# Optimization experiments

Hardware: AMD Instinct MI355X
Metric: run time of the kernel (lower is better)

## Reference

```python
import jax, jax.numpy as jnp
import numpy as np

B, T, E, H = 2, 2048, 1024, 16
D = E // H
K_KEEP = 391
RECENCY = 64
SCALE = D ** -0.5


def setup_inputs() -> dict:
    key = jax.random.key(0)
    k1, k2, k3 = jax.random.split(key, 3)
    x = jax.random.normal(k1, (B, T, E), jnp.float32)
    W_attn = jax.random.normal(k2, (3 * E, E), jnp.float32) * 0.02  # torch Linear weight [out,in]
    W_proj = jax.random.normal(k3, (E, E), jnp.float32) * 0.02
    return {"x": x, "W_attn": W_attn, "W_proj": W_proj}


def reference(x, W_attn, W_proj):
    b, t, c = x.shape
    qkv = x @ W_attn.T                      # [B,T,3E]
    q, k, v = jnp.split(qkv, 3, axis=-1)
    to_heads = lambda u: u.reshape(b, t, H, D).transpose(0, 2, 1, 3)  # [B,H,T,D]
    q, k, v = to_heads(q), to_heads(k), to_heads(v)

    # first pass: causal attention weights for importance scoring
    scores = jnp.einsum('bhqd,bhkd->bhqk', q, k) * SCALE
    causal = jnp.tril(jnp.ones((t, t), dtype=bool))
    scores = jnp.where(causal, scores, -jnp.inf)
    attn_w = jax.nn.softmax(scores, axis=-1)

    # mean importance over query dim, force-keep recent tokens
    imp = attn_w.mean(axis=2)               # [B,H,T]
    imp = imp.at[:, :, -RECENCY:].set(1.0)

    # top-k token selection per (batch, head)
    _, idx = jax.lax.top_k(imp, K_KEEP)     # [B,H,K]

    # gather pruned K/V
    K_keep = jnp.take_along_axis(k, idx[..., None], axis=2)  # [B,H,K,D]
    V_keep = jnp.take_along_axis(v, idx[..., None], axis=2)

    # second attention pass over pruned keys (no causal mask, matches legacy code)
    s2 = jnp.einsum('bhqd,bhkd->bhqk', q, K_keep) * SCALE
    a2 = jax.nn.softmax(s2, axis=-1)
    out = jnp.einsum('bhqk,bhkd->bhqd', a2, V_keep)          # [B,H,T,D]

    out = out.transpose(0, 2, 1, 3).reshape(b, t, c)
    return out @ W_proj.T
```

## Files before the change

kernel.cpp:

```cpp
#include <hip/hip_runtime.h>
#include <hip/hip_bf16.h>


#define TT 2048
#define EE 1024
#define HH 16
#define DD 64
#define KKEEP 391
#define REC 64
#define NBH 32
#define QSCALE 0.125f
#define KPAD 448

typedef short bf16x8 __attribute__((ext_vector_type(8)));
typedef _Float16 f16x8 __attribute__((ext_vector_type(8)));
typedef float f32x4 __attribute__((ext_vector_type(4)));

#define WAIT_VM(N) asm volatile("s_waitcnt vmcnt(" #N ")" ::: "memory")
#define WAIT_LGKM0 asm volatile("s_waitcnt lgkmcnt(0)" ::: "memory")
#define BAR() __builtin_amdgcn_s_barrier()

static __device__ inline unsigned short bf_rn(float x) {
  unsigned u = __float_as_uint(x);
  unsigned r = u + 0x7fffu + ((u >> 16) & 1u);
  return (unsigned short)(r >> 16);
}
static __device__ inline float bf_up(unsigned short h) {
  return __uint_as_float((unsigned)h << 16);
}
static __device__ inline unsigned pkf16(float a, float b) {
  union { _Float16 h[2]; unsigned u; } t;
  t.h[0] = (_Float16)a; t.h[1] = (_Float16)b; return t.u;
}
static __device__ inline void glds16(const void* g, void* l) {
  __builtin_amdgcn_global_load_lds(
      (const __attribute__((address_space(1))) void*)g,
      (__attribute__((address_space(3))) void*)l, 16, 0, 0);
}

static __device__ inline void split4(const float* __restrict__ src,
                                     unsigned short* __restrict__ ho,
                                     unsigned short* __restrict__ lo_, int i)
{
  float4 v = *reinterpret_cast<const float4*>(&src[i]);
  ushort4 hh, ll;
  float f;
  hh.x = bf_rn(v.x); f = bf_up(hh.x); ll.x = bf_rn(v.x - f);
  hh.y = bf_rn(v.y); f = bf_up(hh.y); ll.y = bf_rn(v.y - f);
  hh.z = bf_rn(v.z); f = bf_up(hh.z); ll.z = bf_rn(v.z - f);
  hh.w = bf_rn(v.w); f = bf_up(hh.w); ll.w = bf_rn(v.w - f);
  *reinterpret_cast<ushort4*>(&ho[i]) = hh;
  *reinterpret_cast<ushort4*>(&lo_[i]) = ll;
}

__global__ __launch_bounds__(256) void split_kernel(
    const float* __restrict__ src, unsigned short* __restrict__ ho,
    unsigned short* __restrict__ lo_, int n)
{
  int i = (blockIdx.x * 256 + threadIdx.x) * 4;
  const int stride = gridDim.x * 1024;
  for (; i < n; i += stride) split4(src, ho, lo_, i);
}

__global__ __launch_bounds__(256) void split2_kernel(
    const float* __restrict__ x, const float* __restrict__ wa,
    unsigned short* __restrict__ xh, unsigned short* __restrict__ xl,
    unsigned short* __restrict__ wh, unsigned short* __restrict__ wl)
{
  const int n1 = 4096 * 1024, n2 = 3072 * 1024;
  int i = (blockIdx.x * 256 + threadIdx.x) * 4;
  const int stride = gridDim.x * 1024;
  for (; i < n1 + n2; i += stride) {
    if (i < n1) split4(x, xh, xl, i);
    else        split4(wa, wh, wl, i - n1);
  }
}

template<bool VB, int MODE>
__global__ __launch_bounds__(256) void gemm_pipe(
    const unsigned short* __restrict__ Ah, const unsigned short* __restrict__ Al,
    const unsigned short* __restrict__ Bh, const unsigned short* __restrict__ Bl,
    float* __restrict__ Cc, unsigned short* __restrict__ Qho, unsigned short* __restrict__ Qlo,
    unsigned short* __restrict__ Kho, unsigned short* __restrict__ Klo,
    float* __restrict__ Vo, int M, int N, int Kd, int nOff)
{
  __shared__ __align__(16) unsigned short Ahs[2][128 * 32];
  __shared__ __align__(16) unsigned short Bhs[2][128 * 32];
  __shared__ __align__(16) unsigned short Als[VB ? 1 : 2][128 * 32];
  __shared__ __align__(16) unsigned short Bls[VB ? 1 : 2][128 * 32];
  const int tid = threadIdx.x;
  const int m0 = blockIdx.y * 128, n0 = nOff + blockIdx.x * 128;
  const int w = tid >> 6, lane = tid & 63;
  const int wm = w >> 1, wn = w & 1;
  const int l15 = lane & 15, l4 = lane >> 4;

  size_t gA[2], gB[2]; int ldso[2];
#pragma unroll
  for (int s = 0; s < 2; s++) {
    int seg = w * 2 + s;
    int r = seg * 16 + (lane >> 2);
    int kb = (lane & 3) ^ ((r >> 1) & 3);
    gA[s] = (size_t)(m0 + r) * Kd + kb * 8;
    gB[s] = (size_t)(n0 + r) * Kd + kb * 8;
    ldso[s] = seg * 512;
  }
  auto STAGE = [&](int bb, int k0) {
#pragma unroll
    for (int s = 0; s < 2; s++) {
      glds16(&Ah[gA[s] + k0], &Ahs[bb][ldso[s]]);
      glds16(&Bh[gB[s] + k0], &Bhs[bb][ldso[s]]);
      if (!VB) {
        glds16(&Al[gA[s] + k0], &Als[bb][ldso[s]]);
        glds16(&Bl[gB[s] + k0], &Bls[bb][ldso[s]]);
      }
    }
  };

  f32x4 acc[4][4] = {};

  STAGE(0, 0);
  STAGE(1, 32);
  int cur = 0;
  for (int k0 = 0; k0 < Kd; k0 += 32) {
    if (k0 + 32 < Kd) { if (VB) WAIT_VM(4); else WAIT_VM(8); }
    else WAIT_VM(0);
    BAR();
    bf16x8 ah[4], al[4], bh[4], bl[4];
#pragma unroll
    for (int i = 0; i < 4; i++) {
      int ar = wm * 64 + i * 16 + l15;
      int aoff = ar * 32 + ((l4 ^ ((ar >> 1) & 3)) * 8);
      ah[i] = *reinterpret_cast<const bf16x8*>(&Ahs[cur][aoff]);
      int br = wn * 64 + i * 16 + l15;
      int boff = br * 32 + ((l4 ^ ((br >> 1) & 3)) * 8);
      bh[i] = *reinterpret_cast<const bf16x8*>(&Bhs[cur][boff]);
      if (!VB) {
        al[i] = *reinterpret_cast<const bf16x8*>(&Als[cur][aoff]);
        bl[i] = *reinterpret_cast<const bf16x8*>(&Bls[cur][boff]);
      }
    }
#pragma unroll
    for (int i = 0; i < 4; i++)
#pragma unroll
      for (int j = 0; j < 4; j++) {
        acc[i][j] = __builtin_amdgcn_mfma_f32_16x16x32_bf16(ah[i], bh[j], acc[i][j], 0, 0, 0);
        if (!VB) {
          acc[i][j] = __builtin_amdgcn_mfma_f32_16x16x32_bf16(ah[i], bl[j], acc[i][j], 0, 0, 0);
          acc[i][j] = __builtin_amdgcn_mfma_f32_16x16x32_bf16(al[i], bh[j], acc[i][j], 0, 0, 0);
        }
      }
    WAIT_LGKM0;
    BAR();
    if (k0 + 64 < Kd) STAGE(cur, k0 + 64);
    cur ^= 1;
  }

  if (MODE == 0) {
#pragma unroll
    for (int i = 0; i < 4; i++) {
      int mrow0 = m0 + wm * 64 + i * 16 + l4 * 4;
#pragma unroll
      for (int j = 0; j < 4; j++) {
        int ncol = n0 + wn * 64 + j * 16 + l15;
#pragma unroll
        for (int r = 0; r < 4; r++)
          Cc[(size_t)(mrow0 + r) * N + ncol] = acc[i][j][r];
      }
    }
  } else if (VB) {
#pragma unroll
    for (int j = 0; j < 4; j++) {
      int n = n0 + wn * 64 + j * 16 + l15;
      int rr = n & 1023;
      int h = rr >> 6, d0 = rr & 63;
#pragma unroll
      for (int i = 0; i < 4; i++) {
        int mrow0 = m0 + wm * 64 + i * 16 + l4 * 4;
#pragma unroll
        for (int r = 0; r < 4; r++) {
          int m = mrow0 + r;
          int b = m >> 11, t = m & 2047;
          Vo[((size_t)((b * HH + h) * TT + t)) * DD + d0] = acc[i][j][r];
        }
      }
    }
  } else {
#pragma unroll
    for (int j = 0; j < 4; j++) {
      int n = n0 + wn * 64 + j * 16 + l15;
      int p = n >> 10, rr = n & 1023;
      int h = rr >> 6, d0 = rr & 63;
#pragma unroll
      for (int i = 0; i < 4; i++) {
        int mrow0 = m0 + wm * 64 + i * 16 + l4 * 4;
#pragma unroll
        for (int r = 0; r < 4; r++) {
          int m = mrow0 + r;
          int b = m >> 11, t = m & 2047;
          size_t idx = ((size_t)((b * HH + h) * TT + t)) * DD + d0;
          float v = acc[i][j][r];
          unsigned short hi_ = bf_rn(v);
          unsigned short lo2 = bf_rn(v - bf_up(hi_));
          if (p == 0) { Qho[idx] = hi_; Qlo[idx] = lo2; }
          else        { Kho[idx] = hi_; Klo[idx] = lo2; }
        }
      }
    }
  }
}

__global__ __launch_bounds__(512) void importance5_kernel(
    const unsigned short* __restrict__ Qh, const unsigned short* __restrict__ Ql,
    const unsigned short* __restrict__ Kh, const unsigned short* __restrict__ Kl,
    float* __restrict__ part)
{
  const int bh = blockIdx.x;
  const int rt = blockIdx.z ? (15 - (int)blockIdx.y) : (int)blockIdx.y;
  const int slab = ((int)blockIdx.y << 1) | (int)blockIdx.z;
  const int row0 = rt * 128;
  const int nch = rt + 1;
  const int tid = threadIdx.x;
  const int w = tid >> 6, lane = tid & 63;
  const int wm = w >> 1, wn = w & 1;
  const int l15 = lane & 15, l4 = lane >> 4;
  __shared__ __align__(16) unsigned short Khs[2][128 * 64];
  __shared__ __align__(16) unsigned short Kls[2][128 * 64];
  __shared__ float csw[8 * 128];
  __shared__ float rsb[2 * 128];

  int krow[2], kkb[2], klds[2];
#pragma unroll
  for (int s = 0; s < 2; s++) {
    int seg = w * 2 + s;
    int r = seg * 8 + (lane >> 3);
    int k8 = lane & 7;
    krow[s] = r; kkb[s] = k8 ^ (r & 7); klds[s] = seg * 512;
  }
  auto STAGEK1 = [&](int bb, int ci) {
#pragma unroll
    for (int s = 0; s < 2; s++) {
      size_t ga = ((size_t)(bh * TT + ci * 128 + krow[s])) * DD + kkb[s] * 8;
      glds16(&Kh[ga], &Khs[bb][klds[s]]);
    }
  };
  auto STAGEK2 = [&](int bb, int ci) {
#pragma unroll
    for (int s = 0; s < 2; s++) {
      size_t ga = ((size_t)(bh * TT + ci * 128 + krow[s])) * DD + kkb[s] * 8;
      glds16(&Kh[ga], &Khs[bb][klds[s]]);
      glds16(&Kl[ga], &Kls[bb][klds[s]]);
    }
  };

  bf16x8 aq[2][2], aql[2][2];
#pragma unroll
  for (int ks = 0; ks < 2; ks++)
#pragma unroll
    for (int i = 0; i < 2; i++) {
      int ar = wm * 32 + i * 16 + l15;
      size_t ga = ((size_t)(bh * TT + row0 + ar)) * DD + (ks * 4 + l4) * 8;
      aq[ks][i]  = *reinterpret_cast<const bf16x8*>(&Qh[ga]);
      aql[ks][i] = *reinterpret_cast<const bf16x8*>(&Ql[ga]);
    }

  float rsum[2][4];
#pragma unroll
  for (int i = 0; i < 2; i++)
#pragma unroll
    for (int r = 0; r < 4; r++) rsum[i][r] = 0.f;
  float invl[2][4];

  STAGEK1(0, 0);
  if (nch > 1) STAGEK1(1, 1);
  int cur = 0;
  for (int ci = 0; ci < nch; ci++) {
    if (ci + 1 < nch) WAIT_VM(2); else WAIT_VM(0);
    BAR();
    f32x4 acc[2][4] = {};
#pragma unroll
    for (int ks = 0; ks < 2; ks++) {
#pragma unroll
      for (int j = 0; j < 4; j++) {
        int br = wn * 64 + j * 16 + l15;
        int off = br * 64 + (((ks * 4 + l4) ^ (br & 7)) * 8);
        bf16x8 bh_ = *reinterpret_cast<const bf16x8*>(&Khs[cur][off]);
#pragma unroll
        for (int i = 0; i < 2; i++)
          acc[i][j] = __builtin_amdgcn_mfma_f32_16x16x32_bf16(aq[ks][i], bh_, acc[i][j], 0, 0, 0);
      }
    }
    const bool diag = (ci == rt);
#pragma unroll
    for (int i = 0; i < 2; i++)
#pragma unroll
      for (int r = 0; r < 4; r++) {
        int row = row0 + wm * 32 + i * 16 + l4 * 4 + r;
        float s = 0.f;
#pragma unroll
        for (int j = 0; j < 4; j++) {
          int key = ci * 128 + wn * 64 + j * 16 + l15;
          float p = __expf(acc[i][j][r] * QSCALE);
          if (diag && key > row) p = 0.f;
          s += p;
        }
        rsum[i][r] += s;
      }
    WAIT_LGKM0;
    BAR();
    if (ci + 2 < nch) STAGEK1(cur, ci + 2);
    cur ^= 1;
  }
#pragma unroll
  for (int i = 0; i < 2; i++)
#pragma unroll
    for (int r = 0; r < 4; r++) {
      float v = rsum[i][r];
      v += __shfl_xor(v, 1); v += __shfl_xor(v, 2);
      v += __shfl_xor(v, 4); v += __shfl_xor(v, 8);
      rsum[i][r] = v;
    }
  __syncthreads();
  if (l15 == 0) {
#pragma unroll
    for (int i = 0; i < 2; i++)
#pragma unroll
      for (int r = 0; r < 4; r++)
        rsb[wn * 128 + wm * 32 + i * 16 + l4 * 4 + r] = rsum[i][r];
  }
  __syncthreads();
#pragma unroll
  for (int i = 0; i < 2; i++)
#pragma unroll
    for (int r = 0; r < 4; r++) {
      int rl = wm * 32 + i * 16 + l4 * 4 + r;
      invl[i][r] = 1.0f / (rsb[rl] + rsb[128 + rl]);
    }

  STAGEK2(0, 0);
  if (nch > 1) STAGEK2(1, 1);
  cur = 0;
  for (int ci = 0; ci < nch; ci++) {
    if (ci + 1 < nch) WAIT_VM(4); else WAIT_VM(0);
    BAR();
    f32x4 acc[2][4] = {};
#pragma unroll
    for (int ks = 0; ks < 2; ks++) {
#pragma unroll
      for (int j = 0; j < 4; j++) {
        int br = wn * 64 + j * 16 + l15;
        int off = br * 64 + (((ks * 4 + l4) ^ (br & 7)) * 8);
        bf16x8 bh_ = *reinterpret_cast<const bf16x8*>(&Khs[cur][off]);
        bf16x8 bl_ = *reinterpret_cast<const bf16x8*>(&Kls[cur][off]);
#pragma unroll
        for (int i = 0; i < 2; i++) {
          acc[i][j] = __builtin_amdgcn_mfma_f32_16x16x32_bf16(aq[ks][i], bh_, acc[i][j], 0, 0, 0);
          acc[i][j] = __builtin_amdgcn_mfma_f32_16x16x32_bf16(aq[ks][i], bl_, acc[i][j], 0, 0, 0);
          acc[i][j] = __builtin_amdgcn_mfma_f32_16x16x32_bf16(aql[ks][i], bh_, acc[i][j], 0, 0, 0);
        }
      }
    }
    const bool diag = (ci == rt);
    float cp[4];
#pragma unroll
    for (int j = 0; j < 4; j++) cp[j] = 0.f;
#pragma unroll
    for (int i = 0; i < 2; i++)
#pragma unroll
      for (int r = 0; r < 4; r++) {
        int row = row0 + wm * 32 + i * 16 + l4 * 4 + r;
        float il = invl[i][r];
#pragma unroll
        for (int j = 0; j < 4; j++) {
          int key = ci * 128 + wn * 64 + j * 16 + l15;
          float p = __expf(acc[i][j][r] * QSCALE) * il;
          if (diag && key > row) p = 0.f;
          cp[j] += p;
        }
      }
#pragma unroll
    for (int j = 0; j < 4; j++) {
      float v = cp[j];
      v += __shfl_xor(v, 16); v += __shfl_xor(v, 32);
      cp[j] = v;
    }
    WAIT_LGKM0;
    BAR();
    if (ci + 2 < nch) STAGEK2(cur, ci + 2);
    if (l4 == 0) {
#pragma unroll
      for (int j = 0; j < 4; j++)
        csw[w * 128 + wn * 64 + j * 16 + l15] = cp[j];
    }
    WAIT_LGKM0;
    BAR();
    if (tid < 128) {
      int wnc = tid >> 6;
      float s = csw[(0 * 2 + wnc) * 128 + tid] + csw[(1 * 2 + wnc) * 128 + tid] +
                csw[(2 * 2 + wnc) * 128 + tid] + csw[(3 * 2 + wnc) * 128 + tid];
      part[((size_t)(bh * 16 + slab)) * 2048 + ci * 128 + tid] = s;
    }
    cur ^= 1;
  }
}

__global__ __launch_bounds__(256) void topk_gather_kernel(
    const float* __restrict__ part,
    const unsigned short* __restrict__ Kh, const unsigned short* __restrict__ Kl,
    const float* __restrict__ V,
    unsigned short* __restrict__ Kf, unsigned short* __restrict__ Vt)
{
  const int bh = blockIdx.x, tid = threadIdx.x;
  const int lane = tid & 63, w = tid >> 6;
  __shared__ int redi[4];
  __shared__ int stot;
  __shared__ int base[256];
  __shared__ int idxb[KKEEP];
  unsigned u[8];
#pragma unroll
  for (int k = 0; k < 8; k++) {
    int e = tid * 8 + k;
    float s = 0.f;
#pragma unroll
    for (int p = 0; p < 16; p++) {
      int rtp = (p & 1) ? 15 - (p >> 1) : (p >> 1);
      if (e < (rtp + 1) * 128) s += part[((size_t)(bh * 16 + p)) * 2048 + e];
    }
    float v = (e >= TT - REC) ? 3.0e3f : s;
    u[k] = __float_as_uint(v);
  }
  unsigned lo = 0u, hi = 0x7f800000u;
  for (int it = 0; it < 31; it++) {
    unsigned mid = lo + ((hi - lo + 1) >> 1);
    int c = 0;
#pragma unroll
    for (int k = 0; k < 8; k++) c += (u[k] >= mid) ? 1 : 0;
#pragma unroll
    for (int off = 1; off <= 32; off <<= 1) c += __shfl_xor(c, off);
    if (lane == 0) redi[w] = c;
    __syncthreads();
    int tot = redi[0] + redi[1] + redi[2] + redi[3];
    if (tot >= KKEEP) lo = mid; else hi = mid - 1;
    __syncthreads();
  }
  const unsigned vstar = lo;
  int cgt = 0, ceq = 0;
#pragma unroll
  for (int k = 0; k < 8; k++) { cgt += (u[k] > vstar) ? 1 : 0; ceq += (u[k] == vstar) ? 1 : 0; }
  base[tid] = cgt; __syncthreads();
  if (tid == 0) {
    int run = 0;
    for (int i = 0; i < 256; i++) { int t = base[i]; base[i] = run; run += t; }
    stot = run;
  }
  __syncthreads();
  int off1 = base[tid];
#pragma unroll
  for (int k = 0; k < 8; k++)
    if (u[k] > vstar) idxb[off1++] = tid * 8 + k;
  __syncthreads();
  base[tid] = ceq; __syncthreads();
  if (tid == 0) {
    int run = 0;
    for (int i = 0; i < 256; i++) { int t = base[i]; base[i] = run; run += t; }
  }
  __syncthreads();
  int off2 = stot + base[tid];
#pragma unroll
  for (int k = 0; k < 8; k++)
    if (u[k] == vstar) { if (off2 < KKEEP) idxb[off2] = tid * 8 + k; off2++; }
  __syncthreads();
  for (int f = tid; f < KPAD * 8; f += 256) {
    int kk = f >> 3, c8 = f & 7;
    union { _Float16 h[8]; uint4 v; } o;
#pragma unroll
    for (int j = 0; j < 8; j++) o.h[j] = (_Float16)0.f;
    if (kk < KKEEP) {
      int sr = idxb[kk];
      bf16x8 hv = *reinterpret_cast<const bf16x8*>(&Kh[((size_t)(bh * TT + sr)) * DD + c8 * 8]);
      bf16x8 lv = *reinterpret_cast<const bf16x8*>(&Kl[((size_t)(bh * TT + sr)) * DD + c8 * 8]);
#pragma unroll
      for (int j = 0; j < 8; j++)
        o.h[j] = (_Float16)(bf_up((unsigned short)hv[j]) + bf_up((unsigned short)lv[j]));
    }
    *reinterpret_cast<uint4*>(&Kf[((size_t)(bh * KPAD) + kk) * DD + c8 * 8]) = o.v;
  }
  for (int f = tid; f < KPAD * 8; f += 256) {
    int kk = f >> 3, d8 = f & 7;
    float vv[8];
#pragma unroll
    for (int j = 0; j < 8; j++) vv[j] = 0.f;
    if (kk < KKEEP) {
      int sr = idxb[kk];
      float4 a = *reinterpret_cast<const float4*>(&V[((size_t)(bh * TT + sr)) * DD + d8 * 8]);
      float4 b = *reinterpret_cast<const float4*>(&V[((size_t)(bh * TT + sr)) * DD + d8 * 8 + 4]);
      vv[0] = a.x; vv[1] = a.y; vv[2] = a.z; vv[3] = a.w;
      vv[4] = b.x; vv[5] = b.y; vv[6] = b.z; vv[7] = b.w;
    }
#pragma unroll
    for (int j = 0; j < 8; j++) {
      union { _Float16 h; unsigned short s; } t;
      t.h = (_Float16)vv[j];
      Vt[((size_t)(bh * DD) + d8 * 8 + j) * KPAD + kk] = t.s;
    }
  }
}

__global__ __launch_bounds__(256) void attn4_kernel(
    const unsigned short* __restrict__ Qh, const unsigned short* __restrict__ Ql,
    const unsigned short* __restrict__ Kf, const unsigned short* __restrict__ Vt,
    unsigned short* __restrict__ AOh, unsigned short* __restrict__ AOl)
{
  const int rt = blockIdx.y, bh = blockIdx.x;
  const int tid = threadIdx.x;
  const int w = tid >> 6, lane = tid & 63;
  const int l15 = lane & 15, l4 = lane >> 4;
  __shared__ __align__(16) unsigned short Qs[64 * 64];
  __shared__ __align__(16) unsigned short Ks[2][64 * 64];
  __shared__ __align__(16) unsigned short Vs[2][64 * 64];
  __shared__ float LDSo[4][64][16];
  const int row0 = rt * 64;

  int srow[2], skb[2], slds[2];
#pragma unroll
  for (int s = 0; s < 2; s++) {
    int seg = w * 2 + s;
    int r = seg * 8 + (lane >> 3);
    int k8 = lane & 7;
    srow[s] = r; skb[s] = k8 ^ (r & 7); slds[s] = seg * 512;
  }
  auto STAGEA = [&](int bb, int ci) {
#pragma unroll
    for (int s = 0; s < 2; s++) {
      glds16(&Kf[((size_t)(bh * KPAD) + ci * 64 + srow[s]) * DD + skb[s] * 8], &Ks[bb][slds[s]]);
      glds16(&Vt[((size_t)(bh * DD) + srow[s]) * KPAD + ci * 64 + skb[s] * 8], &Vs[bb][slds[s]]);
    }
  };

#pragma unroll
  for (int it = 0; it < 2; it++) {
    int idx = it * 256 + tid;
    int r = idx >> 3, k8 = idx & 7;
    size_t ga = ((size_t)(bh * TT + row0 + r)) * DD + k8 * 8;
    bf16x8 hv = *reinterpret_cast<const bf16x8*>(&Qh[ga]);
    bf16x8 lv = *reinterpret_cast<const bf16x8*>(&Ql[ga]);
    union { _Float16 h[8]; uint4 v; } q16;
#pragma unroll
    for (int j = 0; j < 8; j++)
      q16.h[j] = (_Float16)(bf_up((unsigned short)hv[j]) + bf_up((unsigned short)lv[j]));
    *reinterpret_cast<uint4*>(&Qs[r * 64 + ((k8 ^ (r & 7)) * 8)]) = q16.v;
  }
  STAGEA(0, 0);
  STAGEA(1, 1);
  WAIT_LGKM0;
  BAR();
  f16x8 bq[2];
#pragma unroll
  for (int ks = 0; ks < 2; ks++) {
    int br = w * 16 + l15;
    bq[ks] = *reinterpret_cast<const f16x8*>(&Qs[br * 64 + (((ks * 4 + l4) ^ (br & 7)) * 8)]);
  }

  f32x4 acc_o[4] = {};
  float rsum = 0.f;
  int cur = 0;

  for (int ci = 0; ci < 7; ci++) {
    if (ci + 1 < 7) WAIT_VM(4); else WAIT_VM(0);
    BAR();
    f32x4 accs[4] = {};
#pragma unroll
    for (int ks = 0; ks < 2; ks++) {
#pragma unroll
      for (int i = 0; i < 4; i++) {
        int kr = i * 16 + l15;
        f16x8 af = *reinterpret_cast<const f16x8*>(&Ks[cur][kr * 64 + (((ks * 4 + l4) ^ (kr & 7)) * 8)]);
        accs[i] = __builtin_amdgcn_mfma_f32_16x16x32_f16(af, bq[ks], accs[i], 0, 0, 0);
      }
    }
    float p[4][4];
#pragma unroll
    for (int i = 0; i < 4; i++)
#pragma unroll
      for (int r = 0; r < 4; r++) {
        int gk = ci * 64 + i * 16 + l4 * 4 + r;
        float pp = __expf(accs[i][r] * QSCALE);
        if (gk >= KKEEP) pp = 0.f;
        p[i][r] = pp;
        rsum += pp;
      }
    unsigned pkU[4][2];
#pragma unroll
    for (int i = 0; i < 4; i++) {
      pkU[i][0] = pkf16(p[i][0], p[i][1]);
      pkU[i][1] = pkf16(p[i][2], p[i][3]);
    }
#pragma unroll
    for (int ks = 0; ks < 2; ks++) {
      union { f16x8 h; unsigned u[4]; } bp;
#pragma unroll
      for (int wp = 0; wp < 4; wp++) {
        int src = ((l4 & 1) * 2 + (wp >> 1)) * 16 + l15;
        unsigned v0 = (unsigned)__shfl((int)pkU[ks * 2][wp & 1], src);
        unsigned v1 = (unsigned)__shfl((int)pkU[ks * 2 + 1][wp & 1], src);
        bp.u[wp] = (l4 & 2) ? v1 : v0;
      }
#pragma unroll
      for (int i = 0; i < 4; i++) {
        int dr = i * 16 + l15;
        f16x8 av = *reinterpret_cast<const f16x8*>(&Vs[cur][dr * 64 + (((ks * 4 + l4) ^ (dr & 7)) * 8)]);
        acc_o[i] = __builtin_amdgcn_mfma_f32_16x16x32_f16(av, bp.h, acc_o[i], 0, 0, 0);
      }
    }
    WAIT_LGKM0;
    BAR();
    if (ci + 2 < 7) STAGEA(cur, ci + 2);
    cur ^= 1;
  }
  rsum += __shfl_xor(rsum, 16);
  rsum += __shfl_xor(rsum, 32);
  float inv = 1.0f / rsum;
#pragma unroll
  for (int i = 0; i < 4; i++)
#pragma unroll
    for (int r = 0; r < 4; r++)
      LDSo[w][i * 16 + l4 * 4 + r][l15] = acc_o[i][r] * inv;
  __syncthreads();
  const int b = bh >> 4, h = bh & 15;
#pragma unroll
  for (int uu = 0; uu < 2; uu++) {
    int u = uu * 64 + lane;
    int q = u >> 3, dc = u & 7;
    int row = row0 + w * 16 + q;
    union { unsigned short s[8]; uint4 v; } sh, sl;
#pragma unroll
    for (int j = 0; j < 8; j++) {
      float v = LDSo[w][dc * 8 + j][q];
      unsigned short hh = bf_rn(v);
      sh.s[j] = hh;
      sl.s[j] = bf_rn(v - bf_up(hh));
    }
    size_t addr = ((size_t)(b * TT + row)) * EE + h * DD + dc * 8;
    *reinterpret_cast<uint4*>(&AOh[addr]) = sh.v;
    *reinterpret_cast<uint4*>(&AOl[addr]) = sl.v;
  }
}

extern "C" void kernel_launch(void* const* d_in, const int* in_sizes, int n_in,
                              void* d_out, int out_size, void* d_ws, size_t ws_size,
                              hipStream_t stream)
{
  const float* x     = (const float*)d_in[0];
  const float* Wattn = (const float*)d_in[1];
  const float* Wproj = (const float*)d_in[2];
  float* out = (float*)d_out;
  float* ws  = (float*)d_ws;

  const size_t SZQ = (size_t)NBH * TT * DD;
  const size_t SZK = (size_t)NBH * KPAD * DD;
  float* Vb   = ws;
  float* part = Vb + SZQ;
  unsigned short* Kf  = (unsigned short*)(part + (size_t)NBH * 16 * TT);
  unsigned short* Vt  = Kf + SZK;
  unsigned short* Qhp = Vt + SZK;
  unsigned short* Qlp = Qhp + SZQ;
  unsigned short* Khp = Qlp + SZQ;
  unsigned short* Klp = Khp + SZQ;
  unsigned short* xh  = Klp + SZQ;
  unsigned short* xl  = xh + (size_t)4096 * 1024;
  unsigned short* Wh  = xl + (size_t)4096 * 1024;
  unsigned short* Wl  = Wh + (size_t)3072 * 1024;
  unsigned short* AOh = xh;
  unsigned short* AOl = xl;
  unsigned short* Ph  = Wh;
  unsigned short* Pl  = Ph + (size_t)1024 * 1024;

  const size_t needB =
      ((size_t)SZQ + (size_t)NBH * 16 * TT) * 4 +
      ((size_t)2 * SZK + (size_t)4 * SZQ + (size_t)2 * 4096 * 1024 + (size_t)2 * 3072 * 1024) * 2;
  if (ws_size < needB) return;

  split2_kernel<<<1024, 256, 0, stream>>>(x, Wattn, xh, xl, Wh, Wl);
  gemm_pipe<false, 1><<<dim3(16, 32), 256, 0, stream>>>(xh, xl, Wh, Wl, nullptr,
      Qhp, Qlp, Khp, Klp, nullptr, 4096, 3072, 1024, 0);
  gemm_pipe<true, 1><<<dim3(8, 32), 256, 0, stream>>>(xh, xl, Wh, Wl, nullptr,
      nullptr, nullptr, nullptr, nullptr, Vb, 4096, 3072, 1024, 2048);
  split_kernel<<<256, 256, 0, stream>>>(Wproj, Ph, Pl, 1024 * 1024);
  importance5_kernel<<<dim3(NBH, 8, 2), 512, 0, stream>>>(Qhp, Qlp, Khp, Klp, part);
  topk_gather_kernel<<<NBH, 256, 0, stream>>>(part, Khp, Klp, Vb, Kf, Vt);
  attn4_kernel<<<dim3(NBH, 32), 256, 0, stream>>>(Qhp, Qlp, Kf, Vt, AOh, AOl);
  gemm_pipe<false, 0><<<dim3(8, 32), 256, 0, stream>>>(AOh, AOl, Ph, Pl, out,
      nullptr, nullptr, nullptr, nullptr, nullptr, 4096, 1024, 1024, 0);
}
```

Baseline: 261.9 us.

## Merge QKV GEMMs into one 512-thread kernel and shrink importance key chunks

```diff
diff --git a/kernel.cpp b/kernel.cpp
--- a/kernel.cpp
+++ b/kernel.cpp
@@ -76,77 +76,72 @@
   }
 }
 
-template<bool VB, int MODE>
-__global__ __launch_bounds__(256) void gemm_pipe(
+template<int MODE>
+__global__ __launch_bounds__(512, 4) void gemm512(
     const unsigned short* __restrict__ Ah, const unsigned short* __restrict__ Al,
     const unsigned short* __restrict__ Bh, const unsigned short* __restrict__ Bl,
     float* __restrict__ Cc, unsigned short* __restrict__ Qho, unsigned short* __restrict__ Qlo,
     unsigned short* __restrict__ Kho, unsigned short* __restrict__ Klo,
-    float* __restrict__ Vo, int M, int N, int Kd, int nOff)
+    float* __restrict__ Vo, int M, int N, int Kd)
 {
   __shared__ __align__(16) unsigned short Ahs[2][128 * 32];
   __shared__ __align__(16) unsigned short Bhs[2][128 * 32];
-  __shared__ __align__(16) unsigned short Als[VB ? 1 : 2][128 * 32];
-  __shared__ __align__(16) unsigned short Bls[VB ? 1 : 2][128 * 32];
+  __shared__ __align__(16) unsigned short Als[2][128 * 32];
+  __shared__ __align__(16) unsigned short Bls[2][128 * 32];
   const int tid = threadIdx.x;
-  const int m0 = blockIdx.y * 128, n0 = nOff + blockIdx.x * 128;
+  const int m0 = blockIdx.y * 128, n0 = blockIdx.x * 128;
   const int w = tid >> 6, lane = tid & 63;
-  const int wm = w >> 1, wn = w & 1;
+  const int wm = w >> 2, wn = w & 3;
   const int l15 = lane & 15, l4 = lane >> 4;
-
-  size_t gA[2], gB[2]; int ldso[2];
-#pragma unroll
-  for (int s = 0; s < 2; s++) {
-    int seg = w * 2 + s;
-    int r = seg * 16 + (lane >> 2);
-    int kb = (lane & 3) ^ ((r >> 1) & 3);
-    gA[s] = (size_t)(m0 + r) * Kd + kb * 8;
-    gB[s] = (size_t)(n0 + r) * Kd + kb * 8;
-    ldso[s] = seg * 512;
-  }
+  const bool vblk = (MODE == 1) && (blockIdx.x >= 16);
+
+  const int sr = w * 16 + (lane >> 2);
+  const int skb = (lane & 3) ^ ((sr >> 1) & 3);
+  const size_t gA = (size_t)(m0 + sr) * Kd + skb * 8;
+  const size_t gB = (size_t)(n0 + sr) * Kd + skb * 8;
+  const int ldw = w * 512;
+
   auto STAGE = [&](int bb, int k0) {
-#pragma unroll
-    for (int s = 0; s < 2; s++) {
-      glds16(&Ah[gA[s] + k0], &Ahs[bb][ldso[s]]);
-      glds16(&Bh[gB[s] + k0], &Bhs[bb][ldso[s]]);
-      if (!VB) {
-        glds16(&Al[gA[s] + k0], &Als[bb][ldso[s]]);
-        glds16(&Bl[gB[s] + k0], &Bls[bb][ldso[s]]);
-      }
+    glds16(&Ah[gA + k0], &Ahs[bb][ldw]);
+    glds16(&Bh[gB + k0], &Bhs[bb][ldw]);
+    if (!vblk) {
+      glds16(&Al[gA + k0], &Als[bb][ldw]);
+      glds16(&Bl[gB + k0], &Bls[bb][ldw]);
     }
   };
 
-  f32x4 acc[4][4] = {};
+  f32x4 acc[4][2] = {};
 
   STAGE(0, 0);
   STAGE(1, 32);
   int cur = 0;
   for (int k0 = 0; k0 < Kd; k0 += 32) {
-    if (k0 + 32 < Kd) { if (VB) WAIT_VM(4); else WAIT_VM(8); }
+    if (k0 + 32 < Kd) { if (vblk) WAIT_VM(2); else WAIT_VM(4); }
     else WAIT_VM(0);
     BAR();
-    bf16x8 ah[4], al[4], bh[4], bl[4];
+    bf16x8 ahf[4], alf[4], bhf[2], blf[2];
 #pragma unroll
     for (int i = 0; i < 4; i++) {
       int ar = wm * 64 + i * 16 + l15;
       int aoff = ar * 32 + ((l4 ^ ((ar >> 1) & 3)) * 8);
-      ah[i] = *reinterpret_cast<const bf16x8*>(&Ahs[cur][aoff]);
-      int br = wn * 64 + i * 16 + l15;
+      ahf[i] = *reinterpret_cast<const bf16x8*>(&Ahs[cur][aoff]);
+      if (!vblk) alf[i] = *reinterpret_cast<const bf16x8*>(&Als[cur][aoff]);
+    }
+#pragma unroll
+    for (int j = 0; j < 2; j++) {
+      int br = wn * 32 + j * 16 + l15;
       int boff = br * 32 + ((l4 ^ ((br >> 1) & 3)) * 8);
-      bh[i] = *reinterpret_cast<const bf16x8*>(&Bhs[cur][boff]);
-      if (!VB) {
-        al[i] = *reinterpret_cast<const bf16x8*>(&Als[cur][aoff]);
-        bl[i] = *reinterpret_cast<const bf16x8*>(&Bls[cur][boff]);
-      }
+      bhf[j] = *reinterpret_cast<const bf16x8*>(&Bhs[cur][boff]);
+      if (!vblk) blf[j] = *reinterpret_cast<const bf16x8*>(&Bls[cur][boff]);
     }
 #pragma unroll
     for (int i = 0; i < 4; i++)
 #pragma unroll
-      for (int j = 0; j < 4; j++) {
-        acc[i][j] = __builtin_amdgcn_mfma_f32_16x16x32_bf16(ah[i], bh[j], acc[i][j], 0, 0, 0);
-        if (!VB) {
-          acc[i][j] = __builtin_amdgcn_mfma_f32_16x16x32_bf16(ah[i], bl[j], acc[i][j], 0, 0, 0);
-          acc[i][j] = __builtin_amdgcn_mfma_f32_16x16x32_bf16(al[i], bh[j], acc[i][j], 0, 0, 0);
+      for (int j = 0; j < 2; j++) {
+        acc[i][j] = __builtin_amdgcn_mfma_f32_16x16x32_bf16(ahf[i], bhf[j], acc[i][j], 0, 0, 0);
+        if (!vblk) {
+          acc[i][j] = __builtin_amdgcn_mfma_f32_16x16x32_bf16(ahf[i], blf[j], acc[i][j], 0, 0, 0);
+          acc[i][j] = __builtin_amdgcn_mfma_f32_16x16x32_bf16(alf[i], bhf[j], acc[i][j], 0, 0, 0);
         }
       }
     WAIT_LGKM0;
@@ -160,34 +155,17 @@
     for (int i = 0; i < 4; i++) {
       int mrow0 = m0 + wm * 64 + i * 16 + l4 * 4;
 #pragma unroll
-      for (int j = 0; j < 4; j++) {
-        int ncol = n0 + wn * 64 + j * 16 + l15;
+      for (int j = 0; j < 2; j++) {
+        int ncol = n0 + wn * 32 + j * 16 + l15;
 #pragma unroll
         for (int r = 0; r < 4; r++)
           Cc[(size_t)(mrow0 + r) * N + ncol] = acc[i][j][r];
       }
     }
-  } else if (VB) {
-#pragma unroll
-    for (int j = 0; j < 4; j++) {
-      int n = n0 + wn * 64 + j * 16 + l15;
-      int rr = n & 1023;
-      int h = rr >> 6, d0 = rr & 63;
-#pragma unroll
-      for (int i = 0; i < 4; i++) {
-        int mrow0 = m0 + wm * 64 + i * 16 + l4 * 4;
-#pragma unroll
-        for (int r = 0; r < 4; r++) {
-          int m = mrow0 + r;
-          int b = m >> 11, t = m & 2047;
-          Vo[((size_t)((b * HH + h) * TT + t)) * DD + d0] = acc[i][j][r];
-        }
-      }
-    }
   } else {
 #pragma unroll
-    for (int j = 0; j < 4; j++) {
-      int n = n0 + wn * 64 + j * 16 + l15;
+    for (int j = 0; j < 2; j++) {
+      int n = n0 + wn * 32 + j * 16 + l15;
       int p = n >> 10, rr = n & 1023;
       int h = rr >> 6, d0 = rr & 63;
 #pragma unroll
@@ -199,17 +177,21 @@
           int b = m >> 11, t = m & 2047;
           size_t idx = ((size_t)((b * HH + h) * TT + t)) * DD + d0;
           float v = acc[i][j][r];
-          unsigned short hi_ = bf_rn(v);
-          unsigned short lo2 = bf_rn(v - bf_up(hi_));
-          if (p == 0) { Qho[idx] = hi_; Qlo[idx] = lo2; }
-          else        { Kho[idx] = hi_; Klo[idx] = lo2; }
+          if (p == 2) {
+            Vo[idx] = v;
+          } else {
+            unsigned short hi_ = bf_rn(v);
+            unsigned short lo2 = bf_rn(v - bf_up(hi_));
+            if (p == 0) { Qho[idx] = hi_; Qlo[idx] = lo2; }
+            else        { Kho[idx] = hi_; Klo[idx] = lo2; }
+          }
         }
       }
     }
   }
 }
 
-__global__ __launch_bounds__(512) void importance5_kernel(
+__global__ __launch_bounds__(512, 8) void importance6_kernel(
     const unsigned short* __restrict__ Qh, const unsigned short* __restrict__ Ql,
     const unsigned short* __restrict__ Kh, const unsigned short* __restrict__ Kl,
     float* __restrict__ part)
@@ -218,38 +200,26 @@
   const int rt = blockIdx.z ? (15 - (int)blockIdx.y) : (int)blockIdx.y;
   const int slab = ((int)blockIdx.y << 1) | (int)blockIdx.z;
   const int row0 = rt * 128;
-  const int nch = rt + 1;
+  const int nch = 2 * rt + 2;
   const int tid = threadIdx.x;
   const int w = tid >> 6, lane = tid & 63;
   const int wm = w >> 1, wn = w & 1;
   const int l15 = lane & 15, l4 = lane >> 4;
-  __shared__ __align__(16) unsigned short Khs[2][128 * 64];
-  __shared__ __align__(16) unsigned short Kls[2][128 * 64];
-  __shared__ float csw[8 * 128];
+  __shared__ __align__(16) unsigned short Khs[2][64 * 64];
+  __shared__ __align__(16) unsigned short Kls[2][64 * 64];
+  __shared__ float csw[8 * 32];
   __shared__ float rsb[2 * 128];
 
-  int krow[2], kkb[2], klds[2];
-#pragma unroll
-  for (int s = 0; s < 2; s++) {
-    int seg = w * 2 + s;
-    int r = seg * 8 + (lane >> 3);
-    int k8 = lane & 7;
-    krow[s] = r; kkb[s] = k8 ^ (r & 7); klds[s] = seg * 512;
-  }
+  const int kr = w * 8 + (lane >> 3);
+  const int sk8 = (lane & 7) ^ (kr & 7);
+  const int ldw = w * 512;
   auto STAGEK1 = [&](int bb, int ci) {
-#pragma unroll
-    for (int s = 0; s < 2; s++) {
-      size_t ga = ((size_t)(bh * TT + ci * 128 + krow[s])) * DD + kkb[s] * 8;
-      glds16(&Kh[ga], &Khs[bb][klds[s]]);
-    }
+    glds16(&Kh[((size_t)(bh * TT + ci * 64 + kr)) * DD + sk8 * 8], &Khs[bb][ldw]);
   };
   auto STAGEK2 = [&](int bb, int ci) {
-#pragma unroll
-    for (int s = 0; s < 2; s++) {
-      size_t ga = ((size_t)(bh * TT + ci * 128 + krow[s])) * DD + kkb[s] * 8;
-      glds16(&Kh[ga], &Khs[bb][klds[s]]);
-      glds16(&Kl[ga], &Kls[bb][klds[s]]);
-    }
+    size_t ga = ((size_t)(bh * TT + ci * 64 + kr)) * DD + sk8 * 8;
+    glds16(&Kh[ga], &Khs[bb][ldw]);
+    glds16(&Kl[ga], &Kls[bb][ldw]);
   };
 
   bf16x8 aq[2][2], aql[2][2];
@@ -271,17 +241,17 @@
   float invl[2][4];
 
   STAGEK1(0, 0);
-  if (nch > 1) STAGEK1(1, 1);
+  STAGEK1(1, 1);
   int cur = 0;
   for (int ci = 0; ci < nch; ci++) {
-    if (ci + 1 < nch) WAIT_VM(2); else WAIT_VM(0);
-    BAR();
-    f32x4 acc[2][4] = {};
+    if (ci + 1 < nch) WAIT_VM(1); else WAIT_VM(0);
+    BAR();
+    f32x4 acc[2][2] = {};
 #pragma unroll
     for (int ks = 0; ks < 2; ks++) {
 #pragma unroll
-      for (int j = 0; j < 4; j++) {
-        int br = wn * 64 + j * 16 + l15;
+      for (int j = 0; j < 2; j++) {
+        int br = wn * 32 + j * 16 + l15;
         int off = br * 64 + (((ks * 4 + l4) ^ (br & 7)) * 8);
         bf16x8 bh_ = *reinterpret_cast<const bf16x8*>(&Khs[cur][off]);
 #pragma unroll
@@ -289,22 +259,33 @@
           acc[i][j] = __builtin_amdgcn_mfma_f32_16x16x32_bf16(aq[ks][i], bh_, acc[i][j], 0, 0, 0);
       }
     }
-    const bool diag = (ci == rt);
-#pragma unroll
-    for (int i = 0; i < 2; i++)
-#pragma unroll
-      for (int r = 0; r < 4; r++) {
-        int row = row0 + wm * 32 + i * 16 + l4 * 4 + r;
-        float s = 0.f;
-#pragma unroll
-        for (int j = 0; j < 4; j++) {
-          int key = ci * 128 + wn * 64 + j * 16 + l15;
-          float p = __expf(acc[i][j][r] * QSCALE);
-          if (diag && key > row) p = 0.f;
-          s += p;
+    if (ci >= 2 * rt) {
+#pragma unroll
+      for (int i = 0; i < 2; i++)
+#pragma unroll
+        for (int r = 0; r < 4; r++) {
+          int row = row0 + wm * 32 + i * 16 + l4 * 4 + r;
+          float s = 0.f;
+#pragma unroll
+          for (int j = 0; j < 2; j++) {
+            int key = ci * 64 + wn * 32 + j * 16 + l15;
+            float p = __expf(acc[i][j][r] * QSCALE);
+            if (key > row) p = 0.f;
+            s += p;
+          }
+          rsum[i][r] += s;
         }
-        rsum[i][r] += s;
-      }
+    } else {
+#pragma unroll
+      for (int i = 0; i < 2; i++)
+#pragma unroll
+        for (int r = 0; r < 4; r++) {
+          float s = 0.f;
+#pragma unroll
+          for (int j = 0; j < 2; j++) s += __expf(acc[i][j][r] * QSCALE);
+          rsum[i][r] += s;
+        }
+    }
     WAIT_LGKM0;
     BAR();
     if (ci + 2 < nch) STAGEK1(cur, ci + 2);
@@ -337,17 +318,17 @@
     }
 
   STAGEK2(0, 0);
-  if (nch > 1) STAGEK2(1, 1);
+  STAGEK2(1, 1);
   cur = 0;
   for (int ci = 0; ci < nch; ci++) {
-    if (ci + 1 < nch) WAIT_VM(4); else WAIT_VM(0);
-    BAR();
-    f32x4 acc[2][4] = {};
+    if (ci + 1 < nch) WAIT_VM(2); else WAIT_VM(0);
+    BAR();
+    f32x4 acc[2][2] = {};
 #pragma unroll
     for (int ks = 0; ks < 2; ks++) {
 #pragma unroll
-      for (int j = 0; j < 4; j++) {
-        int br = wn * 64 + j * 16 + l15;
+      for (int j = 0; j < 2; j++) {
+        int br = wn * 32 + j * 16 + l15;
         int off = br * 64 + (((ks * 4 + l4) ^ (br & 7)) * 8);
         bf16x8 bh_ = *reinterpret_cast<const bf16x8*>(&Khs[cur][off]);
         bf16x8 bl_ = *reinterpret_cast<const bf16x8*>(&Kls[cur][off]);
@@ -359,26 +340,35 @@
         }
       }
     }
-    const bool diag = (ci == rt);
-    float cp[4];
-#pragma unroll
-    for (int j = 0; j < 4; j++) cp[j] = 0.f;
-#pragma unroll
-    for (int i = 0; i < 2; i++)
-#pragma unroll
-      for (int r = 0; r < 4; r++) {
-        int row = row0 + wm * 32 + i * 16 + l4 * 4 + r;
-        float il = invl[i][r];
-#pragma unroll
-        for (int j = 0; j < 4; j++) {
-          int key = ci * 128 + wn * 64 + j * 16 + l15;
-          float p = __expf(acc[i][j][r] * QSCALE) * il;
-          if (diag && key > row) p = 0.f;
-          cp[j] += p;
+    float cp[2] = {0.f, 0.f};
+    if (ci >= 2 * rt) {
+#pragma unroll
+      for (int i = 0; i < 2; i++)
+#pragma unroll
+        for (int r = 0; r < 4; r++) {
+          int row = row0 + wm * 32 + i * 16 + l4 * 4 + r;
+          float il = invl[i][r];
+#pragma unroll
+          for (int j = 0; j < 2; j++) {
+            int key = ci * 64 + wn * 32 + j * 16 + l15;
+            float p = __expf(acc[i][j][r] * QSCALE) * il;
+            if (key > row) p = 0.f;
+            cp[j] += p;
+          }
         }
-      }
-#pragma unroll
-    for (int j = 0; j < 4; j++) {
+    } else {
+#pragma unroll
+      for (int i = 0; i < 2; i++)
+#pragma unroll
+        for (int r = 0; r < 4; r++) {
+          float il = invl[i][r];
+#pragma unroll
+          for (int j = 0; j < 2; j++)
+            cp[j] += __expf(acc[i][j][r] * QSCALE) * il;
+        }
+    }
+#pragma unroll
+    for (int j = 0; j < 2; j++) {
       float v = cp[j];
       v += __shfl_xor(v, 16); v += __shfl_xor(v, 32);
       cp[j] = v;
@@ -388,16 +378,16 @@
     if (ci + 2 < nch) STAGEK2(cur, ci + 2);
     if (l4 == 0) {
 #pragma unroll
-      for (int j = 0; j < 4; j++)
-        csw[w * 128 + wn * 64 + j * 16 + l15] = cp[j];
+      for (int j = 0; j < 2; j++)
+        csw[w * 32 + j * 16 + l15] = cp[j];
     }
     WAIT_LGKM0;
     BAR();
-    if (tid < 128) {
-      int wnc = tid >> 6;
-      float s = csw[(0 * 2 + wnc) * 128 + tid] + csw[(1 * 2 + wnc) * 128 + tid] +
-                csw[(2 * 2 + wnc) * 128 + tid] + csw[(3 * 2 + wnc) * 128 + tid];
-      part[((size_t)(bh * 16 + slab)) * 2048 + ci * 128 + tid] = s;
+    if (tid < 64) {
+      int wnc = tid >> 5, cl = tid & 31;
+      float s = csw[(0 * 2 + wnc) * 32 + cl] + csw[(1 * 2 + wnc) * 32 + cl] +
+                csw[(2 * 2 + wnc) * 32 + cl] + csw[(3 * 2 + wnc) * 32 + cl];
+      part[((size_t)(bh * 16 + slab)) * 2048 + ci * 64 + tid] = s;
     }
     cur ^= 1;
   }
@@ -680,14 +670,12 @@
   if (ws_size < needB) return;
 
   split2_kernel<<<1024, 256, 0, stream>>>(x, Wattn, xh, xl, Wh, Wl);
-  gemm_pipe<false, 1><<<dim3(16, 32), 256, 0, stream>>>(xh, xl, Wh, Wl, nullptr,
-      Qhp, Qlp, Khp, Klp, nullptr, 4096, 3072, 1024, 0);
-  gemm_pipe<true, 1><<<dim3(8, 32), 256, 0, stream>>>(xh, xl, Wh, Wl, nullptr,
-      nullptr, nullptr, nullptr, nullptr, Vb, 4096, 3072, 1024, 2048);
+  gemm512<1><<<dim3(24, 32), 512, 0, stream>>>(xh, xl, Wh, Wl, nullptr,
+      Qhp, Qlp, Khp, Klp, Vb, 4096, 3072, 1024);
   split_kernel<<<256, 256, 0, stream>>>(Wproj, Ph, Pl, 1024 * 1024);
-  importance5_kernel<<<dim3(NBH, 8, 2), 512, 0, stream>>>(Qhp, Qlp, Khp, Klp, part);
+  importance6_kernel<<<dim3(NBH, 8, 2), 512, 0, stream>>>(Qhp, Qlp, Khp, Klp, part);
   topk_gather_kernel<<<NBH, 256, 0, stream>>>(part, Khp, Klp, Vb, Kf, Vt);
   attn4_kernel<<<dim3(NBH, 32), 256, 0, stream>>>(Qhp, Qlp, Kf, Vt, AOh, AOl);
-  gemm_pipe<false, 0><<<dim3(8, 32), 256, 0, stream>>>(AOh, AOl, Ph, Pl, out,
-      nullptr, nullptr, nullptr, nullptr, nullptr, 4096, 1024, 1024, 0);
-}
+  gemm512<0><<<dim3(8, 32), 512, 0, stream>>>(AOh, AOl, Ph, Pl, out,
+      nullptr, nullptr, nullptr, nullptr, nullptr, 4096, 1024, 1024);
+}
```

After: 353.0 us. 34.8% more time.
